# Optimization experiments

Hardware: AMD Instinct MI355X
Metric: run time of the kernel (lower is better)

Reference implementation:

```python
import jax, jax.numpy as jnp
import numpy as np

N_ATOMS = 500000
N_BONDS = 1000000
MAX_NB = 6
ATOM_FDIM = 133
BOND_FDIM = 14
HIDDEN = 128
MP_DEPTH = 3
ATOMS_PER_MOL = 20


def setup_inputs() -> dict:
    key = jax.random.key(0)
    ks = jax.random.split(key, 12)
    inp = {
        "f_atoms": jax.random.normal(ks[0], (N_ATOMS, ATOM_FDIM), jnp.float32),
        "f_bonds": jax.random.normal(ks[1], (N_BONDS, BOND_FDIM), jnp.float32),
        "Wi_w": jax.random.normal(ks[2], (HIDDEN, ATOM_FDIM), jnp.float32) * 0.05,
        "Wi_b": jax.random.normal(ks[3], (HIDDEN,), jnp.float32) * 0.05,
        "Wh_w": jax.random.normal(ks[4], (HIDDEN, HIDDEN + BOND_FDIM), jnp.float32) * 0.05,
        "Wh_b": jax.random.normal(ks[5], (HIDDEN,), jnp.float32) * 0.05,
        "Wo_w": jax.random.normal(ks[6], (HIDDEN, ATOM_FDIM + HIDDEN), jnp.float32) * 0.05,
        "Wo_b": jax.random.normal(ks[7], (HIDDEN,), jnp.float32) * 0.05,
        "ffn_w": jax.random.normal(ks[8], (1, HIDDEN), jnp.float32) * 0.05,
        "ffn_b": jax.random.normal(ks[9], (1,), jnp.float32) * 0.05,
        "a2a": jax.random.randint(ks[10], (N_ATOMS, MAX_NB), 0, N_ATOMS, jnp.int32),
        "a2b": jax.random.randint(ks[11], (N_ATOMS, MAX_NB), 0, N_BONDS, jnp.int32),
        "atoms_per_mol": ATOMS_PER_MOL,
    }
    return inp


def reference(f_atoms, f_bonds, Wi_w, Wi_b, Wh_w, Wh_b, Wo_w, Wo_b, ffn_w, ffn_b,
              a2a, a2b, atoms_per_mol):
    # W_i + ReLU: initial atom messages
    x = f_atoms @ Wi_w.T + Wi_b                     # [N_atoms, H]
    message = jax.nn.relu(x)
    # pre-aggregate bond features once (constant across depths)
    nei_f_bonds_sum = f_bonds[a2b].sum(axis=1)      # [N_atoms, BOND_FDIM]
    for _ in range(MP_DEPTH - 1):
        # gather neighbor messages and sum (index_select_ND + sum(dim=1));
        # concat(msg_gather, bond_gather).sum(1) == concat(sum(msg), sum(bond))
        nei_a_message = message[a2a].sum(axis=1)    # [N_atoms, H]
        nei = jnp.concatenate([nei_a_message, nei_f_bonds_sum], axis=1)
        message = jax.nn.relu(x + nei @ Wh_w.T + Wh_b)
        # dropout is identity in eval mode
    # final aggregation + W_o
    a_message = message[a2a].sum(axis=1)            # [N_atoms, H]
    a_input = jnp.concatenate([f_atoms, a_message], axis=1)
    atom_hiddens = jax.nn.relu(a_input @ Wo_w.T + Wo_b)
    # max readout per molecule (equal-size a_scope of atoms_per_mol)
    n_atoms, h = atom_hiddens.shape
    mol_vecs = atom_hiddens.reshape(n_atoms // atoms_per_mol, atoms_per_mol, h).max(axis=1)
    # FFN head (NN_depth=1): Dropout (identity) + Linear(H -> 1)
    return mol_vecs @ ffn_w.T + ffn_b               # [n_mols, 1]
```

## Files before the change

### kernel.cpp

```cpp
#include <hip/hip_runtime.h>
#include <hip/hip_bf16.h>

#define N_ATOMS   500000
#define N_BONDS   1000000
#define MAX_NB    6
#define ATOM_FDIM 133
#define BOND_FDIM 14
#define HIDDEN    128
#define N_MOLS    25000
#define APM       20

typedef __attribute__((ext_vector_type(8))) short short8;
typedef __attribute__((ext_vector_type(4))) float f32x4;
typedef unsigned short u16;
typedef unsigned int   u32;

__device__ __forceinline__ float bf2f(u16 u) {
    u32 t = ((u32)u) << 16;
    return __builtin_bit_cast(float, t);
}
__device__ __forceinline__ u16 f2bf(float f) {
    u32 t = __builtin_bit_cast(u32, f);
    t += 0x7FFFu + ((t >> 16) & 1u);
    return (u16)(t >> 16);
}

__device__ __forceinline__ void gl16(const u16* g, u16* l) {
    __builtin_amdgcn_global_load_lds(
        (__attribute__((address_space(1))) void*)(g),
        (__attribute__((address_space(3))) void*)(l), 16, 0, 0);
}

__global__ void prep_weights(const float* __restrict__ Wi, const float* __restrict__ Wh,
                             const float* __restrict__ Wo,
                             u16* __restrict__ Wip, u16* __restrict__ Whp, u16* __restrict__ Wop) {
    int stride = gridDim.x * blockDim.x;
    int tid = blockIdx.x * blockDim.x + threadIdx.x;
    for (int i = tid; i < 128 * 160; i += stride) {
        int r = i / 160, c = i % 160;
        Wip[i] = (c < 133) ? f2bf(Wi[r * 133 + c]) : (u16)0;
        Whp[i] = (c < 142) ? f2bf(Wh[r * 142 + c]) : (u16)0;
    }
    for (int i = tid; i < 128 * 288; i += stride) {
        int r = i / 288, c = i % 288;
        float v = 0.f;
        if (c < 133)      v = Wo[r * 261 + c];
        else if (c >= 160) v = Wo[r * 261 + (c - 27)];
        Wop[i] = f2bf(v);
    }
}

#define CROWS 24
__global__ __launch_bounds__(256) void fa_convert(const float* __restrict__ fa, u16* __restrict__ out) {
    __shared__ float buf[CROWS * 133];
    const long row0 = (long)blockIdx.x * CROWS;
    const int rows = (int)((N_ATOMS - row0) < CROWS ? (N_ATOMS - row0) : CROWS);
    const float* src = fa + row0 * ATOM_FDIM;
    if (rows == CROWS) {
        for (int i = threadIdx.x; i < (CROWS * 133) / 4; i += 256)
            *(float4*)(&buf[i * 4]) = *(const float4*)(src + i * 4);
    } else {
        for (int i = threadIdx.x; i < rows * 133; i += 256) buf[i] = src[i];
    }
    __syncthreads();
    for (int j = threadIdx.x; j < rows * 20; j += 256) {
        int r = j / 20, c8 = (j % 20) * 8;
        u16 u[8];
#pragma unroll
        for (int e = 0; e < 8; e++) {
            int c = c8 + e;
            u[e] = (c < ATOM_FDIM) ? f2bf(buf[r * 133 + c]) : (u16)0;
        }
        uint4 v;
        v.x = (u32)u[0] | ((u32)u[1] << 16);
        v.y = (u32)u[2] | ((u32)u[3] << 16);
        v.z = (u32)u[4] | ((u32)u[5] << 16);
        v.w = (u32)u[6] | ((u32)u[7] << 16);
        *(uint4*)(out + (row0 + r) * 160 + c8) = v;
    }
}

__global__ __launch_bounds__(256) void bond_gather(const float* __restrict__ fb, const int* __restrict__ a2b,
                                                   u16* __restrict__ outp) {
    long t = (long)blockIdx.x * 256 + threadIdx.x;
    int atom = (int)(t >> 4);
    int c2   = (int)(t & 15);
    if (atom >= N_ATOMS) return;
    int c0 = 2 * c2, c1 = c0 + 1;
    float s0 = 0.f, s1 = 0.f;
    if (c0 < BOND_FDIM) {
#pragma unroll
        for (int j = 0; j < MAX_NB; j++) {
            int idx = a2b[atom * 6 + j];
            const float* row = fb + (long)idx * BOND_FDIM;
            s0 += row[c0];
            if (c1 < BOND_FDIM) s1 += row[c1];
        }
    }
    *(u32*)(outp + (long)atom * 32 + c0) = (u32)f2bf(s0) | ((u32)f2bf(s1) << 16);
}

__global__ __launch_bounds__(256) void gather_relu_sum(const u16* __restrict__ src,
                                                       const int* __restrict__ a2a,
                                                       u16* __restrict__ dst) {
    long t = (long)blockIdx.x * 256 + threadIdx.x;
    int atom = (int)(t >> 4);
    int c8   = (int)(t & 15) << 3;
    float s[8] = {0, 0, 0, 0, 0, 0, 0, 0};
#pragma unroll
    for (int j = 0; j < MAX_NB; j++) {
        int idx = a2a[atom * 6 + j];
        uint4 v = *(const uint4*)(src + (long)idx * 128 + c8);
        u32 w[4] = {v.x, v.y, v.z, v.w};
#pragma unroll
        for (int q = 0; q < 4; q++) {
            s[2 * q]     += fmaxf(__builtin_bit_cast(float, w[q] << 16), 0.f);
            s[2 * q + 1] += fmaxf(__builtin_bit_cast(float, w[q] & 0xFFFF0000u), 0.f);
        }
    }
    uint4 o;
    o.x = (u32)f2bf(s[0]) | ((u32)f2bf(s[1]) << 16);
    o.y = (u32)f2bf(s[2]) | ((u32)f2bf(s[3]) << 16);
    o.z = (u32)f2bf(s[4]) | ((u32)f2bf(s[5]) << 16);
    o.w = (u32)f2bf(s[6]) | ((u32)f2bf(s[7]) << 16);
    *(uint4*)(dst + (long)atom * 128 + c8) = o;
}

template <int KB0, int KB1, bool ADDX, int WAVES>
__global__ __launch_bounds__(WAVES * 64, 2) void gemm_pp(
    const u16* __restrict__ A0, int ldA0,
    const u16* __restrict__ A1, int ldA1,
    const u16* __restrict__ Wp, const float* __restrict__ bias,
    const u16* __restrict__ Xadd, u16* __restrict__ Out) {
    constexpr int KB   = KB0 + KB1;
    constexpr int KP   = KB * 32;
    constexpr int TILE = WAVES * 16;
    constexpr long NT  = (N_ATOMS + TILE - 1) / TILE;
    constexpr int WSLOTS = KB * 8;
    constexpr int ASLOTS = 2 * WAVES * KB;
    constexpr int XSLOTS = ADDX ? 2 * WAVES * 4 : 0;
    constexpr int NVM  = KB + (ADDX ? 4 : 0);
    __shared__ __align__(16) u16 lds[(WSLOTS + ASLOTS + XSLOTS) * 512];

    const int lane = threadIdx.x & 63;
    const int wave = threadIdx.x >> 6;
    const int lrow = lane & 15;
    const int kg   = lane >> 4;

    u16* WL = lds;
    u16* AL = lds + WSLOTS * 512;
    u16* XL = lds + (WSLOTS + ASLOTS) * 512;

    for (int s = wave; s < WSLOTS; s += WAVES) {
        int kb = s >> 3, n = s & 7;
        gl16(Wp + (n * 16 + lrow) * KP + kb * 32 + kg * 8, WL + s * 512);
    }
    asm volatile("s_waitcnt vmcnt(0)" ::: "memory");
    __syncthreads();

    float4 b4[8];
#pragma unroll
    for (int n = 0; n < 8; n++) b4[n] = *(const float4*)(bias + n * 16 + kg * 4);

    const int G = gridDim.x;

    auto stage = [&](int buf, long t) {
        long row0w = t * TILE + wave * 16;
        long r = row0w + lrow;
        if (r >= N_ATOMS) r = N_ATOMS - 1;
        u16* ab = AL + (buf * WAVES + wave) * KB * 512;
        if constexpr (KB0 > 0) {
            const u16* p = A0 + r * ldA0 + kg * 8;
#pragma unroll
            for (int kb = 0; kb < KB0; kb++) gl16(p + kb * 32, ab + kb * 512);
        }
        if constexpr (KB1 > 0) {
            const u16* p = A1 + r * ldA1 + kg * 8;
#pragma unroll
            for (int kb = 0; kb < KB1; kb++) gl16(p + kb * 32, ab + (KB0 + kb) * 512);
        }
        if constexpr (ADDX) {
            u16* xbse = XL + (buf * WAVES + wave) * 4 * 512;
#pragma unroll
            for (int j = 0; j < 4; j++) {
                long rx = row0w + j * 4 + (lane >> 4);
                if (rx >= N_ATOMS) rx = N_ATOMS - 1;
                gl16(Xadd + rx * 128 + (lane & 15) * 8, xbse + j * 512);
            }
        }
    };

    int buf = 0;
    long t0 = blockIdx.x;
    stage(0, t0);
    for (long t = t0; t < NT; t += G) {
        long tn = (t + G < NT) ? (t + G) : t;
        stage(buf ^ 1, tn);
        asm volatile("s_waitcnt vmcnt(%0)" :: "n"(NVM) : "memory");
        __builtin_amdgcn_sched_barrier(0);

        const u16* abase = AL + (buf * WAVES + wave) * KB * 512;
        f32x4 acc[8];
#pragma unroll
        for (int n = 0; n < 8; n++) acc[n] = (f32x4){0.f, 0.f, 0.f, 0.f};
#pragma unroll
        for (int kb = 0; kb < KB; kb++) {
            short8 af = *(const short8*)(abase + kb * 512 + lane * 8);
#pragma unroll
            for (int n = 0; n < 8; n++) {
                short8 bf = *(const short8*)(WL + (kb * 8 + n) * 512 + lane * 8);
                acc[n] = __builtin_amdgcn_mfma_f32_16x16x32_bf16(bf, af, acc[n], 0, 0, 0);
            }
        }

        long r = t * TILE + wave * 16 + lrow;
        if (r < N_ATOMS) {
            const u16* xbse = XL + (buf * WAVES + wave) * 4 * 512 +
                              (lrow >> 2) * 512 + (lrow & 3) * 128 + (kg >> 1) * 8 + (kg & 1) * 4;
#pragma unroll
            for (int n = 0; n < 8; n++) {
                float v0 = acc[n][0] + b4[n].x;
                float v1 = acc[n][1] + b4[n].y;
                float v2 = acc[n][2] + b4[n].z;
                float v3 = acc[n][3] + b4[n].w;
                if constexpr (ADDX) {
                    uint2 xr = *(const uint2*)(xbse + n * 16);
                    v0 += __builtin_bit_cast(float, xr.x << 16);
                    v1 += __builtin_bit_cast(float, xr.x & 0xFFFF0000u);
                    v2 += __builtin_bit_cast(float, xr.y << 16);
                    v3 += __builtin_bit_cast(float, xr.y & 0xFFFF0000u);
                }
                uint2 o;
                o.x = (u32)f2bf(v0) | ((u32)f2bf(v1) << 16);
                o.y = (u32)f2bf(v2) | ((u32)f2bf(v3) << 16);
                *(uint2*)(Out + r * 128 + n * 16 + kg * 4) = o;
            }
        }
        buf ^= 1;
    }
}

__global__ __launch_bounds__(256) void readout(const u16* __restrict__ ah,
                                               const float* __restrict__ ffn_w,
                                               const float* __restrict__ ffn_b,
                                               float* __restrict__ out) {
    int mol  = blockIdx.x * 4 + (threadIdx.x >> 6);
    int lane = threadIdx.x & 63;
    if (mol >= N_MOLS) return;
    float m0 = -1e30f, m1 = -1e30f;
    const u16* base = ah + (long)mol * APM * 128 + 2 * lane;
#pragma unroll
    for (int a = 0; a < APM; a++) {
        u32 v = *(const u32*)(base + a * 128);
        m0 = fmaxf(m0, bf2f((u16)(v & 0xFFFFu)));
        m1 = fmaxf(m1, bf2f((u16)(v >> 16)));
    }
    m0 = fmaxf(m0, 0.f);
    m1 = fmaxf(m1, 0.f);
    float p = m0 * ffn_w[2 * lane] + m1 * ffn_w[2 * lane + 1];
#pragma unroll
    for (int off = 32; off > 0; off >>= 1) p += __shfl_down(p, off);
    if (lane == 0) out[mol] = p + ffn_b[0];
}

extern "C" void kernel_launch(void* const* d_in, const int* in_sizes, int n_in,
                              void* d_out, int out_size, void* d_ws, size_t ws_size,
                              hipStream_t stream) {
    const float* f_atoms = (const float*)d_in[0];
    const float* f_bonds = (const float*)d_in[1];
    const float* Wi_w = (const float*)d_in[2];
    const float* Wi_b = (const float*)d_in[3];
    const float* Wh_w = (const float*)d_in[4];
    const float* Wh_b = (const float*)d_in[5];
    const float* Wo_w = (const float*)d_in[6];
    const float* Wo_b = (const float*)d_in[7];
    const float* ffn_w = (const float*)d_in[8];
    const float* ffn_b = (const float*)d_in[9];
    const int* a2a = (const int*)d_in[10];
    const int* a2b = (const int*)d_in[11];
    float* out = (float*)d_out;

    char* ws = (char*)d_ws;
    u16* fa    = (u16*)(ws);
    u16* xb    = (u16*)(ws + 160000000L);
    u16* msgA  = (u16*)(ws + 288000000L);
    u16* msgB  = (u16*)(ws + 416000000L);
    u16* nsum  = (u16*)(ws + 544000000L);
    u16* nbond = (u16*)(ws + 672000000L);
    u16* Wip   = (u16*)(ws + 704000000L);
    u16* Whp   = (u16*)(ws + 704040960L);
    u16* Wop   = (u16*)(ws + 704081920L);

    prep_weights<<<64, 256, 0, stream>>>(Wi_w, Wh_w, Wo_w, Wip, Whp, Wop);
    fa_convert<<<(N_ATOMS + CROWS - 1) / CROWS, 256, 0, stream>>>(f_atoms, fa);
    bond_gather<<<31250, 256, 0, stream>>>(f_bonds, a2b, nbond);

    gemm_pp<5, 0, false, 4><<<512, 256, 0, stream>>>(
        fa, 160, (const u16*)nullptr, 0, Wip, Wi_b, (const u16*)nullptr, xb);

    gather_relu_sum<<<31250, 256, 0, stream>>>(xb, a2a, nsum);
    gemm_pp<4, 1, true, 4><<<256, 256, 0, stream>>>(
        nsum, 128, nbond, 32, Whp, Wh_b, xb, msgA);
    gather_relu_sum<<<31250, 256, 0, stream>>>(msgA, a2a, nsum);
    gemm_pp<4, 1, true, 4><<<256, 256, 0, stream>>>(
        nsum, 128, nbond, 32, Whp, Wh_b, xb, msgB);
    gather_relu_sum<<<31250, 256, 0, stream>>>(msgB, a2a, nsum);
    gemm_pp<5, 4, false, 3><<<256, 192, 0, stream>>>(
        fa, 160, nsum, 128, Wop, Wo_b, (const u16*)nullptr, msgA);

    readout<<<6250, 256, 0, stream>>>(msgA, ffn_w, ffn_b, out);
}
```

Baseline: 885.2 us.

## Split output GEMM in two, move GEMMs to 8 waves, read residual from global

The final W_o GEMM is split into two passes. The first computes f_atoms·Wo1+bias into a scratch buffer; the second computes nsum·Wo2 and adds that buffer back in, using a new BIAS template flag. Removing the LDS staging of the residual input (now read straight from global in the epilogue) and the smaller per-kernel K allow every GEMM to run with 8 waves per block. The cost is an extra bf16 round trip of a 500k×128 intermediate, one more kernel launch, and a wait count tuned on the assumption that stores are counted in vmcnt.

```diff
diff --git a/kernel.cpp b/kernel.cpp
--- a/kernel.cpp
+++ b/kernel.cpp
@@ -33,20 +33,19 @@
 
 __global__ void prep_weights(const float* __restrict__ Wi, const float* __restrict__ Wh,
                              const float* __restrict__ Wo,
-                             u16* __restrict__ Wip, u16* __restrict__ Whp, u16* __restrict__ Wop) {
+                             u16* __restrict__ Wip, u16* __restrict__ Whp,
+                             u16* __restrict__ Wop1, u16* __restrict__ Wop2) {
     int stride = gridDim.x * blockDim.x;
     int tid = blockIdx.x * blockDim.x + threadIdx.x;
     for (int i = tid; i < 128 * 160; i += stride) {
         int r = i / 160, c = i % 160;
-        Wip[i] = (c < 133) ? f2bf(Wi[r * 133 + c]) : (u16)0;
-        Whp[i] = (c < 142) ? f2bf(Wh[r * 142 + c]) : (u16)0;
-    }
-    for (int i = tid; i < 128 * 288; i += stride) {
-        int r = i / 288, c = i % 288;
-        float v = 0.f;
-        if (c < 133)      v = Wo[r * 261 + c];
-        else if (c >= 160) v = Wo[r * 261 + (c - 27)];
-        Wop[i] = f2bf(v);
+        Wip[i]  = (c < 133) ? f2bf(Wi[r * 133 + c]) : (u16)0;
+        Whp[i]  = (c < 142) ? f2bf(Wh[r * 142 + c]) : (u16)0;
+        Wop1[i] = (c < 133) ? f2bf(Wo[r * 261 + c]) : (u16)0;
+    }
+    for (int i = tid; i < 128 * 128; i += stride) {
+        int r = i >> 7, c = i & 127;
+        Wop2[i] = f2bf(Wo[r * 261 + 133 + c]);
     }
 }
 
@@ -126,7 +125,7 @@
     *(uint4*)(dst + (long)atom * 128 + c8) = o;
 }
 
-template <int KB0, int KB1, bool ADDX, int WAVES>
+template <int KB0, int KB1, bool ADDX, bool BIAS, int WAVES>
 __global__ __launch_bounds__(WAVES * 64, 2) void gemm_pp(
     const u16* __restrict__ A0, int ldA0,
     const u16* __restrict__ A1, int ldA1,
@@ -138,9 +137,7 @@
     constexpr long NT  = (N_ATOMS + TILE - 1) / TILE;
     constexpr int WSLOTS = KB * 8;
     constexpr int ASLOTS = 2 * WAVES * KB;
-    constexpr int XSLOTS = ADDX ? 2 * WAVES * 4 : 0;
-    constexpr int NVM  = KB + (ADDX ? 4 : 0);
-    __shared__ __align__(16) u16 lds[(WSLOTS + ASLOTS + XSLOTS) * 512];
+    __shared__ __align__(16) u16 lds[(WSLOTS + ASLOTS) * 512];
 
     const int lane = threadIdx.x & 63;
     const int wave = threadIdx.x >> 6;
@@ -149,7 +146,6 @@
 
     u16* WL = lds;
     u16* AL = lds + WSLOTS * 512;
-    u16* XL = lds + (WSLOTS + ASLOTS) * 512;
 
     for (int s = wave; s < WSLOTS; s += WAVES) {
         int kb = s >> 3, n = s & 7;
@@ -160,15 +156,15 @@
 
     float4 b4[8];
 #pragma unroll
-    for (int n = 0; n < 8; n++) b4[n] = *(const float4*)(bias + n * 16 + kg * 4);
+    for (int n = 0; n < 8; n++)
+        b4[n] = BIAS ? *(const float4*)(bias + n * 16 + kg * 4) : (float4){0.f, 0.f, 0.f, 0.f};
 
     const int G = gridDim.x;
 
-    auto stage = [&](int buf, long t) {
-        long row0w = t * TILE + wave * 16;
-        long r = row0w + lrow;
+    auto stage = [&](int sbuf, long t) {
+        long r = t * TILE + wave * 16 + lrow;
         if (r >= N_ATOMS) r = N_ATOMS - 1;
-        u16* ab = AL + (buf * WAVES + wave) * KB * 512;
+        u16* ab = AL + (sbuf * WAVES + wave) * KB * 512;
         if constexpr (KB0 > 0) {
             const u16* p = A0 + r * ldA0 + kg * 8;
 #pragma unroll
@@ -178,25 +174,17 @@
             const u16* p = A1 + r * ldA1 + kg * 8;
 #pragma unroll
             for (int kb = 0; kb < KB1; kb++) gl16(p + kb * 32, ab + (KB0 + kb) * 512);
-        }
-        if constexpr (ADDX) {
-            u16* xbse = XL + (buf * WAVES + wave) * 4 * 512;
-#pragma unroll
-            for (int j = 0; j < 4; j++) {
-                long rx = row0w + j * 4 + (lane >> 4);
-                if (rx >= N_ATOMS) rx = N_ATOMS - 1;
-                gl16(Xadd + rx * 128 + (lane & 15) * 8, xbse + j * 512);
-            }
         }
     };
 
     int buf = 0;
     long t0 = blockIdx.x;
     stage(0, t0);
+    asm volatile("s_waitcnt vmcnt(0)" ::: "memory");
     for (long t = t0; t < NT; t += G) {
         long tn = (t + G < NT) ? (t + G) : t;
         stage(buf ^ 1, tn);
-        asm volatile("s_waitcnt vmcnt(%0)" :: "n"(NVM) : "memory");
+        asm volatile("s_waitcnt vmcnt(%0)" :: "n"(KB + 8) : "memory");
         __builtin_amdgcn_sched_barrier(0);
 
         const u16* abase = AL + (buf * WAVES + wave) * KB * 512;
@@ -215,8 +203,6 @@
 
         long r = t * TILE + wave * 16 + lrow;
         if (r < N_ATOMS) {
-            const u16* xbse = XL + (buf * WAVES + wave) * 4 * 512 +
-                              (lrow >> 2) * 512 + (lrow & 3) * 128 + (kg >> 1) * 8 + (kg & 1) * 4;
 #pragma unroll
             for (int n = 0; n < 8; n++) {
                 float v0 = acc[n][0] + b4[n].x;
@@ -224,7 +210,7 @@
                 float v2 = acc[n][2] + b4[n].z;
                 float v3 = acc[n][3] + b4[n].w;
                 if constexpr (ADDX) {
-                    uint2 xr = *(const uint2*)(xbse + n * 16);
+                    uint2 xr = *(const uint2*)(Xadd + r * 128 + n * 16 + kg * 4);
                     v0 += __builtin_bit_cast(float, xr.x << 16);
                     v1 += __builtin_bit_cast(float, xr.x & 0xFFFF0000u);
                     v2 += __builtin_bit_cast(float, xr.y << 16);
@@ -289,24 +275,27 @@
     u16* nbond = (u16*)(ws + 672000000L);
     u16* Wip   = (u16*)(ws + 704000000L);
     u16* Whp   = (u16*)(ws + 704040960L);
-    u16* Wop   = (u16*)(ws + 704081920L);
-
-    prep_weights<<<64, 256, 0, stream>>>(Wi_w, Wh_w, Wo_w, Wip, Whp, Wop);
+    u16* Wop1  = (u16*)(ws + 704081920L);
+    u16* Wop2  = (u16*)(ws + 704122880L);
+
+    prep_weights<<<64, 256, 0, stream>>>(Wi_w, Wh_w, Wo_w, Wip, Whp, Wop1, Wop2);
     fa_convert<<<(N_ATOMS + CROWS - 1) / CROWS, 256, 0, stream>>>(f_atoms, fa);
     bond_gather<<<31250, 256, 0, stream>>>(f_bonds, a2b, nbond);
 
-    gemm_pp<5, 0, false, 4><<<512, 256, 0, stream>>>(
+    gemm_pp<5, 0, false, true, 8><<<256, 512, 0, stream>>>(
         fa, 160, (const u16*)nullptr, 0, Wip, Wi_b, (const u16*)nullptr, xb);
 
     gather_relu_sum<<<31250, 256, 0, stream>>>(xb, a2a, nsum);
-    gemm_pp<4, 1, true, 4><<<256, 256, 0, stream>>>(
+    gemm_pp<4, 1, true, true, 8><<<256, 512, 0, stream>>>(
         nsum, 128, nbond, 32, Whp, Wh_b, xb, msgA);
     gather_relu_sum<<<31250, 256, 0, stream>>>(msgA, a2a, nsum);
-    gemm_pp<4, 1, true, 4><<<256, 256, 0, stream>>>(
+    gemm_pp<4, 1, true, true, 8><<<256, 512, 0, stream>>>(
         nsum, 128, nbond, 32, Whp, Wh_b, xb, msgB);
     gather_relu_sum<<<31250, 256, 0, stream>>>(msgB, a2a, nsum);
-    gemm_pp<5, 4, false, 3><<<256, 192, 0, stream>>>(
-        fa, 160, nsum, 128, Wop, Wo_b, (const u16*)nullptr, msgA);
+    gemm_pp<5, 0, false, true, 8><<<256, 512, 0, stream>>>(
+        fa, 160, (const u16*)nullptr, 0, Wop1, Wo_b, (const u16*)nullptr, xb);
+    gemm_pp<4, 0, true, false, 8><<<256, 512, 0, stream>>>(
+        nsum, 128, (const u16*)nullptr, 0, Wop2, (const float*)nullptr, xb, msgA);
 
     readout<<<6250, 256, 0, stream>>>(msgA, ffn_w, ffn_b, out);
 }
```

Result: slower. 984.8 us (+11.2%).

## Replace LDS double-buffered GEMM with register-prefetched multi-depth pipeline

Applied to the files above, without the earlier changes.

The streaming GEMM kernels no longer stage A-rows and the residual X through LDS. They load them straight into registers, with a 3-deep prefetch ring controlled by vmcnt waits. Blocks grow to 8 waves (128-row tiles) with 256 blocks for every GEMM. The goal is to drop the LDS write/read round trip and keep more global loads in flight to hide memory latency, at the cost of much higher register pressure, which could limit occupancy or cause spills (especially with KB=9 for the output GEMM).

```diff
diff --git a/kernel.cpp b/kernel.cpp
--- a/kernel.cpp
+++ b/kernel.cpp
@@ -126,32 +126,49 @@
     *(uint4*)(dst + (long)atom * 128 + c8) = o;
 }
 
-template <int KB0, int KB1, bool ADDX, int WAVES>
-__global__ __launch_bounds__(WAVES * 64, 2) void gemm_pp(
+#define ISSUE_SLOT(d, t)                                                              \
+    do {                                                                              \
+        if ((t) < NT) {                                                               \
+            long r_ = (t) * TILE + wave * 16 + lrow;                                  \
+            if (r_ > N_ATOMS - 1) r_ = N_ATOMS - 1;                                   \
+            if constexpr (KB0 > 0) {                                                  \
+                const u16* p_ = A0 + r_ * (long)ldA0 + kg * 8;                        \
+                _Pragma("unroll") for (int kb = 0; kb < KB0; kb++)                    \
+                    a[d][kb] = *(const uint4*)(p_ + kb * 32);                         \
+            }                                                                         \
+            if constexpr (KB1 > 0) {                                                  \
+                const u16* p_ = A1 + r_ * (long)ldA1 + kg * 8;                        \
+                _Pragma("unroll") for (int kb = 0; kb < KB1; kb++)                    \
+                    a[d][KB0 + kb] = *(const uint4*)(p_ + kb * 32);                   \
+            }                                                                         \
+            if constexpr (ADDX) {                                                     \
+                _Pragma("unroll") for (int n = 0; n < 8; n++)                         \
+                    xv[d][n] = *(const uint2*)(Xadd + r_ * 128 + n * 16 + kg * 4);    \
+            }                                                                         \
+        }                                                                             \
+    } while (0)
+
+template <int KB0, int KB1, bool ADDX, bool BIAS, int DEPTH>
+__global__ __launch_bounds__(512, 2) void gemm_rp(
     const u16* __restrict__ A0, int ldA0,
     const u16* __restrict__ A1, int ldA1,
     const u16* __restrict__ Wp, const float* __restrict__ bias,
     const u16* __restrict__ Xadd, u16* __restrict__ Out) {
-    constexpr int KB   = KB0 + KB1;
-    constexpr int KP   = KB * 32;
-    constexpr int TILE = WAVES * 16;
-    constexpr long NT  = (N_ATOMS + TILE - 1) / TILE;
+    constexpr int KB    = KB0 + KB1;
+    constexpr int KP    = KB * 32;
+    constexpr int TILE  = 128;
+    constexpr long NT   = (N_ATOMS + TILE - 1) / TILE;
     constexpr int WSLOTS = KB * 8;
-    constexpr int ASLOTS = 2 * WAVES * KB;
-    constexpr int XSLOTS = ADDX ? 2 * WAVES * 4 : 0;
-    constexpr int NVM  = KB + (ADDX ? 4 : 0);
-    __shared__ __align__(16) u16 lds[(WSLOTS + ASLOTS + XSLOTS) * 512];
+    constexpr int NWAIT = (DEPTH - 1) * (KB + 8 + (ADDX ? 8 : 0));
+    static_assert(NWAIT <= 63, "vmcnt range");
+    __shared__ __align__(16) u16 WL[WSLOTS * 512];
 
     const int lane = threadIdx.x & 63;
     const int wave = threadIdx.x >> 6;
     const int lrow = lane & 15;
     const int kg   = lane >> 4;
 
-    u16* WL = lds;
-    u16* AL = lds + WSLOTS * 512;
-    u16* XL = lds + (WSLOTS + ASLOTS) * 512;
-
-    for (int s = wave; s < WSLOTS; s += WAVES) {
+    for (int s = wave; s < WSLOTS; s += 8) {
         int kb = s >> 3, n = s & 7;
         gl16(Wp + (n * 16 + lrow) * KP + kb * 32 + kg * 8, WL + s * 512);
     }
@@ -160,83 +177,70 @@
 
     float4 b4[8];
 #pragma unroll
-    for (int n = 0; n < 8; n++) b4[n] = *(const float4*)(bias + n * 16 + kg * 4);
-
-    const int G = gridDim.x;
-
-    auto stage = [&](int buf, long t) {
-        long row0w = t * TILE + wave * 16;
-        long r = row0w + lrow;
-        if (r >= N_ATOMS) r = N_ATOMS - 1;
-        u16* ab = AL + (buf * WAVES + wave) * KB * 512;
-        if constexpr (KB0 > 0) {
-            const u16* p = A0 + r * ldA0 + kg * 8;
-#pragma unroll
-            for (int kb = 0; kb < KB0; kb++) gl16(p + kb * 32, ab + kb * 512);
-        }
-        if constexpr (KB1 > 0) {
-            const u16* p = A1 + r * ldA1 + kg * 8;
-#pragma unroll
-            for (int kb = 0; kb < KB1; kb++) gl16(p + kb * 32, ab + (KB0 + kb) * 512);
-        }
-        if constexpr (ADDX) {
-            u16* xbse = XL + (buf * WAVES + wave) * 4 * 512;
-#pragma unroll
-            for (int j = 0; j < 4; j++) {
-                long rx = row0w + j * 4 + (lane >> 4);
-                if (rx >= N_ATOMS) rx = N_ATOMS - 1;
-                gl16(Xadd + rx * 128 + (lane & 15) * 8, xbse + j * 512);
+    for (int n = 0; n < 8; n++)
+        b4[n] = BIAS ? *(const float4*)(bias + n * 16 + kg * 4) : (float4){0.f, 0.f, 0.f, 0.f};
+
+    const int G  = gridDim.x;
+    const long t0 = blockIdx.x;
+
+    uint4 a[DEPTH][KB];
+    uint2 xv[DEPTH][ADDX ? 8 : 1];
+
+#pragma unroll
+    for (int d = 0; d < DEPTH; d++) {
+        long tp = t0 + (long)d * G;
+        ISSUE_SLOT(d, tp);
+    }
+    __builtin_amdgcn_sched_barrier(0);
+
+#pragma unroll 1
+    for (long tt = t0; tt < NT; tt += (long)DEPTH * G) {
+#pragma unroll
+        for (int d = 0; d < DEPTH; d++) {
+            long t = tt + (long)d * G;
+            if (t < NT) {
+                asm volatile("s_waitcnt vmcnt(%0)" :: "n"(NWAIT) : "memory");
+                __builtin_amdgcn_sched_barrier(0);
+
+                f32x4 acc[8];
+#pragma unroll
+                for (int n = 0; n < 8; n++) acc[n] = (f32x4){0.f, 0.f, 0.f, 0.f};
+#pragma unroll
+                for (int kb = 0; kb < KB; kb++) {
+                    short8 af = __builtin_bit_cast(short8, a[d][kb]);
+#pragma unroll
+                    for (int n = 0; n < 8; n++) {
+                        short8 bf = *(const short8*)(WL + (kb * 8 + n) * 512 + lane * 8);
+                        acc[n] = __builtin_amdgcn_mfma_f32_16x16x32_bf16(bf, af, acc[n], 0, 0, 0);
+                    }
+                }
+
+                long r = t * TILE + wave * 16 + lrow;
+                if (r < N_ATOMS) {
+#pragma unroll
+                    for (int n = 0; n < 8; n++) {
+                        float v0 = acc[n][0] + b4[n].x;
+                        float v1 = acc[n][1] + b4[n].y;
+                        float v2 = acc[n][2] + b4[n].z;
+                        float v3 = acc[n][3] + b4[n].w;
+                        if constexpr (ADDX) {
+                            v0 += __builtin_bit_cast(float, xv[d][n].x << 16);
+                            v1 += __builtin_bit_cast(float, xv[d][n].x & 0xFFFF0000u);
+                            v2 += __builtin_bit_cast(float, xv[d][n].y << 16);
+                            v3 += __builtin_bit_cast(float, xv[d][n].y & 0xFFFF0000u);
+                        }
+                        uint2 o;
+                        o.x = (u32)f2bf(v0) | ((u32)f2bf(v1) << 16);
+                        o.y = (u32)f2bf(v2) | ((u32)f2bf(v3) << 16);
+                        *(uint2*)(Out + r * 128 + n * 16 + kg * 4) = o;
+                    }
+                }
+                __builtin_amdgcn_sched_barrier(0);
+                long tf = t + (long)DEPTH * G;
+                ISSUE_SLOT(d, tf);
+                __builtin_amdgcn_sched_barrier(0);
             }
         }
-    };
-
-    int buf = 0;
-    long t0 = blockIdx.x;
-    stage(0, t0);
-    for (long t = t0; t < NT; t += G) {
-        long tn = (t + G < NT) ? (t + G) : t;
-        stage(buf ^ 1, tn);
-        asm volatile("s_waitcnt vmcnt(%0)" :: "n"(NVM) : "memory");
-        __builtin_amdgcn_sched_barrier(0);
-
-        const u16* abase = AL + (buf * WAVES + wave) * KB * 512;
-        f32x4 acc[8];
-#pragma unroll
-        for (int n = 0; n < 8; n++) acc[n] = (f32x4){0.f, 0.f, 0.f, 0.f};
-#pragma unroll
-        for (int kb = 0; kb < KB; kb++) {
-            short8 af = *(const short8*)(abase + kb * 512 + lane * 8);
-#pragma unroll
-            for (int n = 0; n < 8; n++) {
-                short8 bf = *(const short8*)(WL + (kb * 8 + n) * 512 + lane * 8);
-                acc[n] = __builtin_amdgcn_mfma_f32_16x16x32_bf16(bf, af, acc[n], 0, 0, 0);
-            }
-        }
-
-        long r = t * TILE + wave * 16 + lrow;
-        if (r < N_ATOMS) {
-            const u16* xbse = XL + (buf * WAVES + wave) * 4 * 512 +
-                              (lrow >> 2) * 512 + (lrow & 3) * 128 + (kg >> 1) * 8 + (kg & 1) * 4;
-#pragma unroll
-            for (int n = 0; n < 8; n++) {
-                float v0 = acc[n][0] + b4[n].x;
-                float v1 = acc[n][1] + b4[n].y;
-                float v2 = acc[n][2] + b4[n].z;
-                float v3 = acc[n][3] + b4[n].w;
-                if constexpr (ADDX) {
-                    uint2 xr = *(const uint2*)(xbse + n * 16);
-                    v0 += __builtin_bit_cast(float, xr.x << 16);
-                    v1 += __builtin_bit_cast(float, xr.x & 0xFFFF0000u);
-                    v2 += __builtin_bit_cast(float, xr.y << 16);
-                    v3 += __builtin_bit_cast(float, xr.y & 0xFFFF0000u);
-                }
-                uint2 o;
-                o.x = (u32)f2bf(v0) | ((u32)f2bf(v1) << 16);
-                o.y = (u32)f2bf(v2) | ((u32)f2bf(v3) << 16);
-                *(uint2*)(Out + r * 128 + n * 16 + kg * 4) = o;
-            }
-        }
-        buf ^= 1;
     }
 }
 
@@ -295,17 +299,17 @@
     fa_convert<<<(N_ATOMS + CROWS - 1) / CROWS, 256, 0, stream>>>(f_atoms, fa);
     bond_gather<<<31250, 256, 0, stream>>>(f_bonds, a2b, nbond);
 
-    gemm_pp<5, 0, false, 4><<<512, 256, 0, stream>>>(
+    gemm_rp<5, 0, false, true, 3><<<256, 512, 0, stream>>>(
         fa, 160, (const u16*)nullptr, 0, Wip, Wi_b, (const u16*)nullptr, xb);
 
     gather_relu_sum<<<31250, 256, 0, stream>>>(xb, a2a, nsum);
-    gemm_pp<4, 1, true, 4><<<256, 256, 0, stream>>>(
+    gemm_rp<4, 1, true, true, 3><<<256, 512, 0, stream>>>(
         nsum, 128, nbond, 32, Whp, Wh_b, xb, msgA);
     gather_relu_sum<<<31250, 256, 0, stream>>>(msgA, a2a, nsum);
-    gemm_pp<4, 1, true, 4><<<256, 256, 0, stream>>>(
+    gemm_rp<4, 1, true, true, 3><<<256, 512, 0, stream>>>(
         nsum, 128, nbond, 32, Whp, Wh_b, xb, msgB);
     gather_relu_sum<<<31250, 256, 0, stream>>>(msgB, a2a, nsum);
-    gemm_pp<5, 4, false, 3><<<256, 192, 0, stream>>>(
+    gemm_rp<5, 4, false, true, 3><<<256, 512, 0, stream>>>(
         fa, 160, nsum, 128, Wop, Wo_b, (const u16*)nullptr, msgA);
 
     readout<<<6250, 256, 0, stream>>>(msgA, ffn_w, ffn_b, out);
```

Measured after the change: 897.7 us. No clear change (+1.4%).
